# Performance work log

Hardware: AMD Instinct MI355X
Metric: run time of the kernel (lower is better)

Reference implementation:

```python
import jax, jax.numpy as jnp
import numpy as np

N = 50000      # nodes (cells)
E = 800000     # directed edges
IN, H1, H2, Z = 512, 128, 128, 64


def setup_inputs() -> dict:
    key = jax.random.key(0)
    ks = jax.random.split(key, 12)
    x = jax.random.normal(ks[0], (N, IN), jnp.float32)
    edge_index = jax.random.randint(ks[1], (2, E), 0, N, dtype=jnp.int64)

    def glorot(k, i, o):
        return jax.random.normal(k, (i, o), jnp.float32) * np.float32(1.0 / np.sqrt(i))

    return {
        "x": x,
        "edge_index": edge_index,
        "W1": glorot(ks[2], IN, H1), "b1": jnp.zeros((H1,), jnp.float32),
        "W2": glorot(ks[3], H1, H2), "b2": jnp.zeros((H2,), jnp.float32),
        "Wm": glorot(ks[4], H2, Z),  "bm": jnp.zeros((Z,), jnp.float32),
        "Ws": glorot(ks[5], H2, Z),  "bs": jnp.zeros((Z,), jnp.float32),
    }


def _gcn_norm(edge_index, n):
    # PyG GCNConv default: add self-loops, sym-normalize D^-1/2 (A+I) D^-1/2
    loops = jnp.arange(n, dtype=edge_index.dtype)
    src = jnp.concatenate([edge_index[0], loops])
    dst = jnp.concatenate([edge_index[1], loops])
    deg = jax.ops.segment_sum(jnp.ones_like(dst, jnp.float32), dst, num_segments=n)
    dis = jnp.where(deg > 0, jax.lax.rsqrt(jnp.maximum(deg, 1.0)), 0.0)
    norm = dis[src] * dis[dst]  # [E+N]
    return src, dst, norm


def _gcn_conv(x, W, b, src, dst, norm, n):
    h = x @ W                          # [N, out] transform first
    msg = h[src] * norm[:, None]       # gather + scale
    out = jax.ops.segment_sum(msg, dst, num_segments=n)  # scatter-add at targets
    return out + b


def reference(x, edge_index, W1, b1, W2, b2, Wm, bm, Ws, bs):
    n = x.shape[0]
    src, dst, norm = _gcn_norm(edge_index, n)
    h = jax.nn.relu(_gcn_conv(x, W1, b1, src, dst, norm, n))
    h = jax.nn.relu(_gcn_conv(h, W2, b2, src, dst, norm, n))
    # dropout p=0.4 is identity in eval mode
    z_mean = _gcn_conv(h, Wm, bm, src, dst, norm, n)
    z_log_std = _gcn_conv(h, Ws, bs, src, dst, norm, n)
    return (z_mean, z_log_std)
```

## Files before the change

### kernel.cpp

```cpp
#include <hip/hip_runtime.h>


using u16 = unsigned short;
typedef __attribute__((ext_vector_type(8))) short short8;
typedef __attribute__((ext_vector_type(4))) float f32x4;

__device__ __forceinline__ void split_bf16(float f, u16& hi, u16& lo) {
    unsigned b = __float_as_uint(f);
    hi = (u16)(b >> 16);
    float rem = f - __uint_as_float(b & 0xFFFF0000u);
    lo = (u16)(__float_as_uint(rem) >> 16);
}

__device__ __forceinline__ int block_mode(const int* __restrict__ ew, int* sflag) {
    if (threadIdx.x == 0) *sflag = 0;
    __syncthreads();
    if (ew[2 * (int)threadIdx.x + 1] != 0) atomicOr(sflag, 1);
    __syncthreads();
    return *sflag ? 0 : 1;
}

__global__ void deg_kernel(const int* __restrict__ ew, int* __restrict__ deg, int E) {
    __shared__ int sflag;
    int mode = block_mode(ew, &sflag);
    int e = blockIdx.x * blockDim.x + threadIdx.x;
    if (e >= E) return;
    int d = mode ? ew[2 * E + 2 * e] : ew[E + e];
    atomicAdd(&deg[d], 1);
}

__global__ void scan_block_kernel(const int* __restrict__ deg, int* __restrict__ rowptr,
                                  int* __restrict__ aux, float* __restrict__ dis, int N) {
    __shared__ int s[256];
    int i = blockIdx.x * 256 + threadIdx.x;
    int v = (i < N) ? deg[i] : 0;
    if (i < N) dis[i] = rsqrtf((float)v + 1.0f);
    s[threadIdx.x] = v;
    __syncthreads();
    for (int off = 1; off < 256; off <<= 1) {
        int t = (threadIdx.x >= off) ? s[threadIdx.x - off] : 0;
        __syncthreads();
        s[threadIdx.x] += t;
        __syncthreads();
    }
    if (i < N) rowptr[i] = s[threadIdx.x] - v;
    if (threadIdx.x == 255) aux[blockIdx.x] = s[255];
}

__global__ void scan_aux_kernel(int* __restrict__ aux, int nb) {
    __shared__ int s[256];
    int i = threadIdx.x;
    int v = (i < nb) ? aux[i] : 0;
    s[i] = v;
    __syncthreads();
    for (int off = 1; off < 256; off <<= 1) {
        int t = (i >= off) ? s[i - off] : 0;
        __syncthreads();
        s[i] += t;
        __syncthreads();
    }
    if (i < nb) aux[i] = s[i] - v;
}

__global__ void add_offsets_kernel(int* __restrict__ rowptr, const int* __restrict__ aux,
                                   int N, int E) {
    int i = blockIdx.x * 256 + threadIdx.x;
    if (i < N) rowptr[i] += aux[i >> 8];
    if (i == 0) rowptr[N] = E;
}

__global__ void fill_csr_kernel(const int* __restrict__ ew,
                                const int* __restrict__ rowptr, int* __restrict__ cursor,
                                int* __restrict__ csr_src, int E) {
    __shared__ int sflag;
    int mode = block_mode(ew, &sflag);
    int e = blockIdx.x * blockDim.x + threadIdx.x;
    if (e >= E) return;
    int s = mode ? ew[2 * e] : ew[e];
    int d = mode ? ew[2 * E + 2 * e] : ew[E + e];
    int pos = rowptr[d] + atomicAdd(&cursor[d], 1);
    csr_src[pos] = s;
}

__global__ void conv_all_kernel(const float* __restrict__ W1, const float* __restrict__ W2,
                                const float* __restrict__ Wm, const float* __restrict__ Ws,
                                u16* __restrict__ W1t_hi, u16* __restrict__ W1t_lo,
                                u16* __restrict__ W2t_hi, u16* __restrict__ W2t_lo,
                                u16* __restrict__ Wct_hi, u16* __restrict__ Wct_lo) {
    int idx = blockIdx.x * 256 + threadIdx.x;
    u16 h, l;
    if (idx < 65536) {
        int k = idx >> 7, n = idx & 127;
        split_bf16(W1[idx], h, l);
        W1t_hi[n * 512 + k] = h;
        W1t_lo[n * 512 + k] = l;
    } else if (idx < 81920) {
        int t = idx - 65536;
        int k = t >> 7, n = t & 127;
        split_bf16(W2[t], h, l);
        W2t_hi[n * 128 + k] = h;
        W2t_lo[n * 128 + k] = l;
    } else if (idx < 98304) {
        int t = idx - 81920;
        int k = t >> 7, j = t & 127;
        float f = (j < 64) ? Wm[k * 64 + j] : Ws[k * 64 + (j - 64)];
        split_bf16(f, h, l);
        Wct_hi[j * 128 + k] = h;
        Wct_lo[j * 128 + k] = l;
    }
}

#define TILE_OFF(t) ((t) * 520)

__global__ __launch_bounds__(256) void gemm_mfma(const float* __restrict__ A,
                                                 const u16* __restrict__ Bt_hi,
                                                 const u16* __restrict__ Bt_lo,
                                                 float* __restrict__ C,
                                                 int N, int K) {
    __shared__ u16 AsH[4 * 520], AsL[4 * 520];
    __shared__ u16 BsH[8 * 520], BsL[8 * 520];

    const int tid = threadIdx.x;
    const int w = tid >> 6, lane = tid & 63;
    const int row0 = blockIdx.y * 64;

    const int s_ar = w * 16 + (lane & 15);
    const int s_ak = (lane >> 4) * 8;
    const int a_dst = TILE_OFF(w) + lane * 8;
    const int s_bc = tid >> 1;
    const int s_bk = (tid & 1) * 16;
    const int b_q0 = (tid & 1) * 2;
    const int b_dst0 = TILE_OFF(s_bc >> 4) + ((s_bc & 15) + 16 * (b_q0 + 0)) * 8;
    const int b_dst1 = TILE_OFF(s_bc >> 4) + ((s_bc & 15) + 16 * (b_q0 + 1)) * 8;

    const int R = (w >> 1) * 32, Cc = (w & 1) * 64;
    const int atile = (w >> 1) * 2;
    const int btile = (w & 1) * 4;
    const int m16 = lane & 15, quad = lane >> 4;

    f32x4 acc[2][4];
#pragma unroll
    for (int i = 0; i < 2; ++i)
#pragma unroll
        for (int j = 0; j < 4; ++j) acc[i][j] = (f32x4)0.f;

    const int grow = row0 + s_ar;
    const bool ok = (grow < N);
    const float* aptr = A + (size_t)grow * K + s_ak;
    const u16* bph = Bt_hi + (size_t)s_bc * K + s_bk;
    const u16* bpl = Bt_lo + (size_t)s_bc * K + s_bk;

    float av[8];
    short8 rbh0, rbh1, rbl0, rbl1;
    {
        f32x4 v0 = (f32x4)0.f, v1 = (f32x4)0.f;
        if (ok) { v0 = *(const f32x4*)&aptr[0]; v1 = *(const f32x4*)&aptr[4]; }
#pragma unroll
        for (int q = 0; q < 4; ++q) { av[q] = v0[q]; av[4 + q] = v1[q]; }
        rbh0 = *(const short8*)&bph[0];
        rbh1 = *(const short8*)&bph[8];
        rbl0 = *(const short8*)&bpl[0];
        rbl1 = *(const short8*)&bpl[8];
    }

    const int ksteps = K >> 5;
    for (int ks = 0; ks < ksteps; ++ks) {
        short8 ah, al;
#pragma unroll
        for (int q = 0; q < 8; ++q) {
            u16 h, l;
            split_bf16(av[q], h, l);
            ah[q] = (short)h;
            al[q] = (short)l;
        }
        __syncthreads();
        *(short8*)&AsH[a_dst] = ah;
        *(short8*)&AsL[a_dst] = al;
        *(short8*)&BsH[b_dst0] = rbh0;
        *(short8*)&BsH[b_dst1] = rbh1;
        *(short8*)&BsL[b_dst0] = rbl0;
        *(short8*)&BsL[b_dst1] = rbl1;
        __syncthreads();

        if (ks + 1 < ksteps) {
            const int k0 = (ks + 1) * 32;
            f32x4 v0 = (f32x4)0.f, v1 = (f32x4)0.f;
            if (ok) { v0 = *(const f32x4*)&aptr[k0]; v1 = *(const f32x4*)&aptr[k0 + 4]; }
#pragma unroll
            for (int q = 0; q < 4; ++q) { av[q] = v0[q]; av[4 + q] = v1[q]; }
            rbh0 = *(const short8*)&bph[k0];
            rbh1 = *(const short8*)&bph[k0 + 8];
            rbl0 = *(const short8*)&bpl[k0];
            rbl1 = *(const short8*)&bpl[k0 + 8];
        }

        short8 fa_h[2], fa_l[2], fb_h[4], fb_l[4];
#pragma unroll
        for (int i = 0; i < 2; ++i) {
            fa_h[i] = *(const short8*)&AsH[TILE_OFF(atile + i) + lane * 8];
            fa_l[i] = *(const short8*)&AsL[TILE_OFF(atile + i) + lane * 8];
        }
#pragma unroll
        for (int j = 0; j < 4; ++j) {
            fb_h[j] = *(const short8*)&BsH[TILE_OFF(btile + j) + lane * 8];
            fb_l[j] = *(const short8*)&BsL[TILE_OFF(btile + j) + lane * 8];
        }
#pragma unroll
        for (int i = 0; i < 2; ++i)
#pragma unroll
            for (int j = 0; j < 4; ++j) {
                acc[i][j] = __builtin_amdgcn_mfma_f32_16x16x32_bf16(
                    fa_h[i], fb_h[j], acc[i][j], 0, 0, 0);
                acc[i][j] = __builtin_amdgcn_mfma_f32_16x16x32_bf16(
                    fa_h[i], fb_l[j], acc[i][j], 0, 0, 0);
                acc[i][j] = __builtin_amdgcn_mfma_f32_16x16x32_bf16(
                    fa_l[i], fb_h[j], acc[i][j], 0, 0, 0);
            }
    }

#pragma unroll
    for (int i = 0; i < 2; ++i) {
#pragma unroll
        for (int r = 0; r < 4; ++r) {
            int gr = row0 + R + i * 16 + quad * 4 + r;
            if (gr < N) {
#pragma unroll
                for (int j = 0; j < 4; ++j)
                    C[(size_t)gr * 128 + Cc + j * 16 + m16] = acc[i][j][r];
            }
        }
    }
}

__global__ __launch_bounds__(256) void propagate_kernel(
    const float* __restrict__ h, const int* __restrict__ rowptr,
    const int* __restrict__ csr_src, const float* __restrict__ dis,
    const float* __restrict__ bias, float* __restrict__ out, int N, int do_relu) {
    int wave = (blockIdx.x * 256 + threadIdx.x) >> 6;
    int lane = threadIdx.x & 63;
    if (wave >= N) return;
    int v = wave;
    int f = lane * 2;
    float dv = dis[v];
    float ax = 0.f, ay = 0.f;
    int beg = rowptr[v], end = rowptr[v + 1];
    int i = beg;
    for (; i + 8 <= end; i += 8) {
        int s[8];
        float ww[8];
        float2 g[8];
#pragma unroll
        for (int u = 0; u < 8; ++u) s[u] = csr_src[i + u];
#pragma unroll
        for (int u = 0; u < 8; ++u) ww[u] = dis[s[u]];
#pragma unroll
        for (int u = 0; u < 8; ++u) g[u] = *(const float2*)&h[(size_t)s[u] * 128 + f];
#pragma unroll
        for (int u = 0; u < 8; ++u) {
            float t = ww[u] * dv;
            ax += t * g[u].x;
            ay += t * g[u].y;
        }
    }
    if (i + 4 <= end) {
        int s[4];
        float ww[4];
        float2 g[4];
#pragma unroll
        for (int u = 0; u < 4; ++u) s[u] = csr_src[i + u];
#pragma unroll
        for (int u = 0; u < 4; ++u) ww[u] = dis[s[u]];
#pragma unroll
        for (int u = 0; u < 4; ++u) g[u] = *(const float2*)&h[(size_t)s[u] * 128 + f];
#pragma unroll
        for (int u = 0; u < 4; ++u) {
            float t = ww[u] * dv;
            ax += t * g[u].x;
            ay += t * g[u].y;
        }
        i += 4;
    }
    for (; i < end; ++i) {
        int s = csr_src[i];
        float ws = dis[s] * dv;
        float2 g = *(const float2*)&h[(size_t)s * 128 + f];
        ax += ws * g.x;
        ay += ws * g.y;
    }
    float2 hv = *(const float2*)&h[(size_t)v * 128 + f];
    ax += dv * dv * hv.x;
    ay += dv * dv * hv.y;
    ax += bias[f];
    ay += bias[f + 1];
    if (do_relu) { ax = fmaxf(ax, 0.f); ay = fmaxf(ay, 0.f); }
    *(float2*)&out[(size_t)v * 128 + f] = make_float2(ax, ay);
}

__global__ __launch_bounds__(256) void propagate_final_kernel(
    const float* __restrict__ h, const int* __restrict__ rowptr,
    const int* __restrict__ csr_src, const float* __restrict__ dis,
    const float* __restrict__ bm, const float* __restrict__ bs,
    float* __restrict__ out, int N) {
    int wave = (blockIdx.x * 256 + threadIdx.x) >> 6;
    int lane = threadIdx.x & 63;
    if (wave >= N) return;
    int v = wave;
    int f = lane * 2;
    float dv = dis[v];
    float ax = 0.f, ay = 0.f;
    int beg = rowptr[v], end = rowptr[v + 1];
    int i = beg;
    for (; i + 8 <= end; i += 8) {
        int s[8];
        float ww[8];
        float2 g[8];
#pragma unroll
        for (int u = 0; u < 8; ++u) s[u] = csr_src[i + u];
#pragma unroll
        for (int u = 0; u < 8; ++u) ww[u] = dis[s[u]];
#pragma unroll
        for (int u = 0; u < 8; ++u) g[u] = *(const float2*)&h[(size_t)s[u] * 128 + f];
#pragma unroll
        for (int u = 0; u < 8; ++u) {
            float t = ww[u] * dv;
            ax += t * g[u].x;
            ay += t * g[u].y;
        }
    }
    if (i + 4 <= end) {
        int s[4];
        float ww[4];
        float2 g[4];
#pragma unroll
        for (int u = 0; u < 4; ++u) s[u] = csr_src[i + u];
#pragma unroll
        for (int u = 0; u < 4; ++u) ww[u] = dis[s[u]];
#pragma unroll
        for (int u = 0; u < 4; ++u) g[u] = *(const float2*)&h[(size_t)s[u] * 128 + f];
#pragma unroll
        for (int u = 0; u < 4; ++u) {
            float t = ww[u] * dv;
            ax += t * g[u].x;
            ay += t * g[u].y;
        }
        i += 4;
    }
    for (; i < end; ++i) {
        int s = csr_src[i];
        float ws = dis[s] * dv;
        float2 g = *(const float2*)&h[(size_t)s * 128 + f];
        ax += ws * g.x;
        ay += ws * g.y;
    }
    float2 hv = *(const float2*)&h[(size_t)v * 128 + f];
    ax += dv * dv * hv.x;
    ay += dv * dv * hv.y;
    if (f < 64) {
        *(float2*)&out[(size_t)v * 64 + f] = make_float2(ax + bm[f], ay + bm[f + 1]);
    } else {
        int g = f - 64;
        *(float2*)&out[(size_t)N * 64 + (size_t)v * 64 + g] =
            make_float2(ax + bs[g], ay + bs[g + 1]);
    }
}

extern "C" void kernel_launch(void* const* d_in, const int* in_sizes, int n_in,
                              void* d_out, int out_size, void* d_ws, size_t ws_size,
                              hipStream_t stream) {
    const float* x  = (const float*)d_in[0];
    const int*   ew = (const int*)d_in[1];
    const float* W1 = (const float*)d_in[2];
    const float* b1 = (const float*)d_in[3];
    const float* W2 = (const float*)d_in[4];
    const float* b2 = (const float*)d_in[5];
    const float* Wm = (const float*)d_in[6];
    const float* bm = (const float*)d_in[7];
    const float* Ws = (const float*)d_in[8];
    const float* bs = (const float*)d_in[9];
    float* out = (float*)d_out;

    const int IN = 512, H = 128;
    const int N = in_sizes[0] / IN;
    const int E = in_sizes[1] / 2;

    char* base = (char*)d_ws;
    size_t off = 0;
    auto alloc = [&](size_t bytes) -> char* {
        char* p = base + off;
        off = (off + bytes + 255) & ~(size_t)255;
        return p;
    };
    char*  degcur  = (char*) alloc(400384);
    float* dis     = (float*)alloc((size_t)N * 4);
    int*   rowptr  = (int*)  alloc((size_t)(N + 1) * 4);
    int*   aux     = (int*)  alloc(256 * 4);
    int*   csr_src = (int*)  alloc((size_t)E * 4);
    u16*   W1t_hi  = (u16*)  alloc((size_t)IN * H * 2);
    u16*   W1t_lo  = (u16*)  alloc((size_t)IN * H * 2);
    u16*   W2t_hi  = (u16*)  alloc((size_t)H * H * 2);
    u16*   W2t_lo  = (u16*)  alloc((size_t)H * H * 2);
    u16*   Wct_hi  = (u16*)  alloc((size_t)H * H * 2);
    u16*   Wct_lo  = (u16*)  alloc((size_t)H * H * 2);
    float* hA      = (float*)alloc((size_t)N * H * 4);
    float* hB      = (float*)alloc((size_t)N * H * 4);
    (void)ws_size; (void)n_in; (void)out_size;

    int* deg    = (int*)degcur;
    int* cursor = (int*)(degcur + 200192);

    hipMemsetAsync(degcur, 0, 400384, stream);

    const int eblocks = (E + 255) / 256;
    const int nblocks = (N + 255) / 256;

    conv_all_kernel<<<(98304 + 255) / 256, 256, 0, stream>>>(
        W1, W2, Wm, Ws, W1t_hi, W1t_lo, W2t_hi, W2t_lo, Wct_hi, Wct_lo);
    deg_kernel<<<eblocks, 256, 0, stream>>>(ew, deg, E);
    scan_block_kernel<<<nblocks, 256, 0, stream>>>(deg, rowptr, aux, dis, N);
    scan_aux_kernel<<<1, 256, 0, stream>>>(aux, nblocks);
    add_offsets_kernel<<<nblocks, 256, 0, stream>>>(rowptr, aux, N, E);
    fill_csr_kernel<<<eblocks, 256, 0, stream>>>(ew, rowptr, cursor, csr_src, E);

    dim3 gg(1, (N + 63) / 64);
    const int pblocks = (N * 64 + 255) / 256;

    gemm_mfma<<<gg, 256, 0, stream>>>(x, W1t_hi, W1t_lo, hA, N, IN);
    propagate_kernel<<<pblocks, 256, 0, stream>>>(hA, rowptr, csr_src, dis,
                                                  b1, hB, N, 1);
    gemm_mfma<<<gg, 256, 0, stream>>>(hB, W2t_hi, W2t_lo, hA, N, H);
    propagate_kernel<<<pblocks, 256, 0, stream>>>(hA, rowptr, csr_src, dis,
                                                  b2, hB, N, 1);
    gemm_mfma<<<gg, 256, 0, stream>>>(hB, Wct_hi, Wct_lo, hA, N, H);
    propagate_final_kernel<<<pblocks, 256, 0, stream>>>(hA, rowptr, csr_src, dis,
                                                        bm, bs, out, N);
}
```

Measured before the change: 499.5 us.

## Load GEMM fragments directly from global memory and emit split-bf16 activations from propagate

Replaces the LDS-staged MFMA GEMM with a templated kernel where each wave loads its A and B fragments straight from global memory into registers, with register double-buffering and a fully unrolled K loop. This removes both __syncthreads barriers and the shared-memory traffic. The propagate kernel now applies ReLU and writes the hi/lo bf16 split of its output, so the layer-2 and final GEMMs read pre-split bf16 activations and skip the per-step split work. In exchange, B fragments are re-read from global/L2 by every wave instead of being shared through LDS, and register pressure goes up.

```diff
diff --git a/kernel.cpp b/kernel.cpp
--- a/kernel.cpp
+++ b/kernel.cpp
@@ -110,33 +110,43 @@
     }
 }
 
-#define TILE_OFF(t) ((t) * 520)
-
-__global__ __launch_bounds__(256) void gemm_mfma(const float* __restrict__ A,
-                                                 const u16* __restrict__ Bt_hi,
-                                                 const u16* __restrict__ Bt_lo,
-                                                 float* __restrict__ C,
-                                                 int N, int K) {
-    __shared__ u16 AsH[4 * 520], AsL[4 * 520];
-    __shared__ u16 BsH[8 * 520], BsL[8 * 520];
-
+template <int K, bool SPLIT>
+__global__ __launch_bounds__(256) void gemm_direct(
+    const float* __restrict__ A,
+    const u16* __restrict__ Ahi, const u16* __restrict__ Alo,
+    const u16* __restrict__ Bh, const u16* __restrict__ Bl,
+    float* __restrict__ C, int N) {
     const int tid = threadIdx.x;
     const int w = tid >> 6, lane = tid & 63;
-    const int row0 = blockIdx.y * 64;
-
-    const int s_ar = w * 16 + (lane & 15);
-    const int s_ak = (lane >> 4) * 8;
-    const int a_dst = TILE_OFF(w) + lane * 8;
-    const int s_bc = tid >> 1;
-    const int s_bk = (tid & 1) * 16;
-    const int b_q0 = (tid & 1) * 2;
-    const int b_dst0 = TILE_OFF(s_bc >> 4) + ((s_bc & 15) + 16 * (b_q0 + 0)) * 8;
-    const int b_dst1 = TILE_OFF(s_bc >> 4) + ((s_bc & 15) + 16 * (b_q0 + 1)) * 8;
-
+    const int row0 = blockIdx.x * 64;
     const int R = (w >> 1) * 32, Cc = (w & 1) * 64;
-    const int atile = (w >> 1) * 2;
-    const int btile = (w & 1) * 4;
-    const int m16 = lane & 15, quad = lane >> 4;
+    const int m16 = lane & 15, quad = lane >> 4, kq = quad * 8;
+
+    int r0 = row0 + R + m16;
+    int r1 = r0 + 16;
+    if (r0 > N - 1) r0 = N - 1;
+    if (r1 > N - 1) r1 = N - 1;
+
+    const float* a0;
+    const float* a1;
+    const u16 *ah0, *ah1, *al0, *al1;
+    if constexpr (SPLIT) {
+        ah0 = Ahi + (size_t)r0 * K + kq;
+        ah1 = Ahi + (size_t)r1 * K + kq;
+        al0 = Alo + (size_t)r0 * K + kq;
+        al1 = Alo + (size_t)r1 * K + kq;
+    } else {
+        a0 = A + (size_t)r0 * K + kq;
+        a1 = A + (size_t)r1 * K + kq;
+    }
+    const u16* bhp[4];
+    const u16* blp[4];
+#pragma unroll
+    for (int j = 0; j < 4; ++j) {
+        int n = Cc + j * 16 + m16;
+        bhp[j] = Bh + (size_t)n * K + kq;
+        blp[j] = Bl + (size_t)n * K + kq;
+    }
 
     f32x4 acc[2][4];
 #pragma unroll
@@ -144,78 +154,100 @@
 #pragma unroll
         for (int j = 0; j < 4; ++j) acc[i][j] = (f32x4)0.f;
 
-    const int grow = row0 + s_ar;
-    const bool ok = (grow < N);
-    const float* aptr = A + (size_t)grow * K + s_ak;
-    const u16* bph = Bt_hi + (size_t)s_bc * K + s_bk;
-    const u16* bpl = Bt_lo + (size_t)s_bc * K + s_bk;
-
-    float av[8];
-    short8 rbh0, rbh1, rbl0, rbl1;
-    {
-        f32x4 v0 = (f32x4)0.f, v1 = (f32x4)0.f;
-        if (ok) { v0 = *(const f32x4*)&aptr[0]; v1 = *(const f32x4*)&aptr[4]; }
-#pragma unroll
-        for (int q = 0; q < 4; ++q) { av[q] = v0[q]; av[4 + q] = v1[q]; }
-        rbh0 = *(const short8*)&bph[0];
-        rbh1 = *(const short8*)&bph[8];
-        rbl0 = *(const short8*)&bpl[0];
-        rbl1 = *(const short8*)&bpl[8];
-    }
-
-    const int ksteps = K >> 5;
-    for (int ks = 0; ks < ksteps; ++ks) {
-        short8 ah, al;
-#pragma unroll
-        for (int q = 0; q < 8; ++q) {
-            u16 h, l;
-            split_bf16(av[q], h, l);
-            ah[q] = (short)h;
-            al[q] = (short)l;
-        }
-        __syncthreads();
-        *(short8*)&AsH[a_dst] = ah;
-        *(short8*)&AsL[a_dst] = al;
-        *(short8*)&BsH[b_dst0] = rbh0;
-        *(short8*)&BsH[b_dst1] = rbh1;
-        *(short8*)&BsL[b_dst0] = rbl0;
-        *(short8*)&BsL[b_dst1] = rbl1;
-        __syncthreads();
-
-        if (ks + 1 < ksteps) {
-            const int k0 = (ks + 1) * 32;
-            f32x4 v0 = (f32x4)0.f, v1 = (f32x4)0.f;
-            if (ok) { v0 = *(const f32x4*)&aptr[k0]; v1 = *(const f32x4*)&aptr[k0 + 4]; }
-#pragma unroll
-            for (int q = 0; q < 4; ++q) { av[q] = v0[q]; av[4 + q] = v1[q]; }
-            rbh0 = *(const short8*)&bph[k0];
-            rbh1 = *(const short8*)&bph[k0 + 8];
-            rbl0 = *(const short8*)&bpl[k0];
-            rbl1 = *(const short8*)&bpl[k0 + 8];
-        }
-
-        short8 fa_h[2], fa_l[2], fb_h[4], fb_l[4];
-#pragma unroll
-        for (int i = 0; i < 2; ++i) {
-            fa_h[i] = *(const short8*)&AsH[TILE_OFF(atile + i) + lane * 8];
-            fa_l[i] = *(const short8*)&AsL[TILE_OFF(atile + i) + lane * 8];
-        }
-#pragma unroll
-        for (int j = 0; j < 4; ++j) {
-            fb_h[j] = *(const short8*)&BsH[TILE_OFF(btile + j) + lane * 8];
-            fb_l[j] = *(const short8*)&BsL[TILE_OFF(btile + j) + lane * 8];
-        }
+    float curA[2][8];
+    short8 curAh[2], curAl[2];
+    short8 curBh[4], curBl[4];
+
+    if constexpr (SPLIT) {
+        curAh[0] = *(const short8*)&ah0[0];
+        curAh[1] = *(const short8*)&ah1[0];
+        curAl[0] = *(const short8*)&al0[0];
+        curAl[1] = *(const short8*)&al1[0];
+    } else {
+        f32x4 v00 = *(const f32x4*)&a0[0], v01 = *(const f32x4*)&a0[4];
+        f32x4 v10 = *(const f32x4*)&a1[0], v11 = *(const f32x4*)&a1[4];
+#pragma unroll
+        for (int q = 0; q < 4; ++q) {
+            curA[0][q] = v00[q]; curA[0][4 + q] = v01[q];
+            curA[1][q] = v10[q]; curA[1][4 + q] = v11[q];
+        }
+    }
+#pragma unroll
+    for (int j = 0; j < 4; ++j) {
+        curBh[j] = *(const short8*)&bhp[j][0];
+        curBl[j] = *(const short8*)&blp[j][0];
+    }
+
+    const int NSTEP = K / 32;
+#pragma unroll
+    for (int ks = 0; ks < NSTEP; ++ks) {
+        float nxtA[2][8];
+        short8 nxtAh[2], nxtAl[2], nxtBh[4], nxtBl[4];
+        const bool more = (ks + 1 < NSTEP);
+        if (more) {
+            const int kb = (ks + 1) * 32;
+            if constexpr (SPLIT) {
+                nxtAh[0] = *(const short8*)&ah0[kb];
+                nxtAh[1] = *(const short8*)&ah1[kb];
+                nxtAl[0] = *(const short8*)&al0[kb];
+                nxtAl[1] = *(const short8*)&al1[kb];
+            } else {
+                f32x4 v00 = *(const f32x4*)&a0[kb], v01 = *(const f32x4*)&a0[kb + 4];
+                f32x4 v10 = *(const f32x4*)&a1[kb], v11 = *(const f32x4*)&a1[kb + 4];
+#pragma unroll
+                for (int q = 0; q < 4; ++q) {
+                    nxtA[0][q] = v00[q]; nxtA[0][4 + q] = v01[q];
+                    nxtA[1][q] = v10[q]; nxtA[1][4 + q] = v11[q];
+                }
+            }
+#pragma unroll
+            for (int j = 0; j < 4; ++j) {
+                nxtBh[j] = *(const short8*)&bhp[j][kb];
+                nxtBl[j] = *(const short8*)&blp[j][kb];
+            }
+        }
+
+        short8 ah[2], al[2];
+        if constexpr (SPLIT) {
+#pragma unroll
+            for (int i = 0; i < 2; ++i) { ah[i] = curAh[i]; al[i] = curAl[i]; }
+        } else {
+#pragma unroll
+            for (int i = 0; i < 2; ++i)
+#pragma unroll
+                for (int q = 0; q < 8; ++q) {
+                    u16 h, l;
+                    split_bf16(curA[i][q], h, l);
+                    ah[i][q] = (short)h;
+                    al[i][q] = (short)l;
+                }
+        }
+
 #pragma unroll
         for (int i = 0; i < 2; ++i)
 #pragma unroll
             for (int j = 0; j < 4; ++j) {
                 acc[i][j] = __builtin_amdgcn_mfma_f32_16x16x32_bf16(
-                    fa_h[i], fb_h[j], acc[i][j], 0, 0, 0);
+                    ah[i], curBh[j], acc[i][j], 0, 0, 0);
                 acc[i][j] = __builtin_amdgcn_mfma_f32_16x16x32_bf16(
-                    fa_h[i], fb_l[j], acc[i][j], 0, 0, 0);
+                    ah[i], curBl[j], acc[i][j], 0, 0, 0);
                 acc[i][j] = __builtin_amdgcn_mfma_f32_16x16x32_bf16(
-                    fa_l[i], fb_h[j], acc[i][j], 0, 0, 0);
+                    al[i], curBh[j], acc[i][j], 0, 0, 0);
             }
+
+        if (more) {
+            if constexpr (SPLIT) {
+#pragma unroll
+                for (int i = 0; i < 2; ++i) { curAh[i] = nxtAh[i]; curAl[i] = nxtAl[i]; }
+            } else {
+#pragma unroll
+                for (int i = 0; i < 2; ++i)
+#pragma unroll
+                    for (int q = 0; q < 8; ++q) curA[i][q] = nxtA[i][q];
+            }
+#pragma unroll
+            for (int j = 0; j < 4; ++j) { curBh[j] = nxtBh[j]; curBl[j] = nxtBl[j]; }
+        }
     }
 
 #pragma unroll
@@ -235,7 +267,8 @@
 __global__ __launch_bounds__(256) void propagate_kernel(
     const float* __restrict__ h, const int* __restrict__ rowptr,
     const int* __restrict__ csr_src, const float* __restrict__ dis,
-    const float* __restrict__ bias, float* __restrict__ out, int N, int do_relu) {
+    const float* __restrict__ bias, u16* __restrict__ out_hi,
+    u16* __restrict__ out_lo, int N) {
     int wave = (blockIdx.x * 256 + threadIdx.x) >> 6;
     int lane = threadIdx.x & 63;
     if (wave >= N) return;
@@ -292,8 +325,13 @@
     ay += dv * dv * hv.y;
     ax += bias[f];
     ay += bias[f + 1];
-    if (do_relu) { ax = fmaxf(ax, 0.f); ay = fmaxf(ay, 0.f); }
-    *(float2*)&out[(size_t)v * 128 + f] = make_float2(ax, ay);
+    ax = fmaxf(ax, 0.f);
+    ay = fmaxf(ay, 0.f);
+    u16 hx, lx, hy, ly;
+    split_bf16(ax, hx, lx);
+    split_bf16(ay, hy, ly);
+    *(ushort2*)&out_hi[(size_t)v * 128 + f] = make_ushort2(hx, hy);
+    *(ushort2*)&out_lo[(size_t)v * 128 + f] = make_ushort2(lx, ly);
 }
 
 __global__ __launch_bounds__(256) void propagate_final_kernel(
@@ -402,7 +440,8 @@
     u16*   Wct_hi  = (u16*)  alloc((size_t)H * H * 2);
     u16*   Wct_lo  = (u16*)  alloc((size_t)H * H * 2);
     float* hA      = (float*)alloc((size_t)N * H * 4);
-    float* hB      = (float*)alloc((size_t)N * H * 4);
+    u16*   hBhi    = (u16*)  alloc((size_t)N * H * 2);
+    u16*   hBlo    = (u16*)  alloc((size_t)N * H * 2);
     (void)ws_size; (void)n_in; (void)out_size;
 
     int* deg    = (int*)degcur;
@@ -421,16 +460,19 @@
     add_offsets_kernel<<<nblocks, 256, 0, stream>>>(rowptr, aux, N, E);
     fill_csr_kernel<<<eblocks, 256, 0, stream>>>(ew, rowptr, cursor, csr_src, E);
 
-    dim3 gg(1, (N + 63) / 64);
+    const int gblocks = (N + 63) / 64;
     const int pblocks = (N * 64 + 255) / 256;
 
-    gemm_mfma<<<gg, 256, 0, stream>>>(x, W1t_hi, W1t_lo, hA, N, IN);
+    gemm_direct<512, false><<<gblocks, 256, 0, stream>>>(
+        x, nullptr, nullptr, W1t_hi, W1t_lo, hA, N);
     propagate_kernel<<<pblocks, 256, 0, stream>>>(hA, rowptr, csr_src, dis,
-                                                  b1, hB, N, 1);
-    gemm_mfma<<<gg, 256, 0, stream>>>(hB, W2t_hi, W2t_lo, hA, N, H);
+                                                  b1, hBhi, hBlo, N);
+    gemm_direct<128, true><<<gblocks, 256, 0, stream>>>(
+        nullptr, hBhi, hBlo, W2t_hi, W2t_lo, hA, N);
     propagate_kernel<<<pblocks, 256, 0, stream>>>(hA, rowptr, csr_src, dis,
-                                                  b2, hB, N, 1);
-    gemm_mfma<<<gg, 256, 0, stream>>>(hB, Wct_hi, Wct_lo, hA, N, H);
+                                                  b2, hBhi, hBlo, N);
+    gemm_direct<128, true><<<gblocks, 256, 0, stream>>>(
+        nullptr, hBhi, hBlo, Wct_hi, Wct_lo, hA, N);
     propagate_final_kernel<<<pblocks, 256, 0, stream>>>(hA, rowptr, csr_src, dis,
                                                         bm, bs, out, N);
 }
```

Measured after the change: 561.2 us. 12.4% more time.
